# Kernel tuning notes

Hardware: AMD Instinct MI355X
Metric: run time of the kernel (lower is better)

## Reference

```python
import jax, jax.numpy as jnp
import numpy as np

N = 100000        # nodes
E = 1600000       # edges (avg degree 16)
D1, D2 = 512, 256 # omic feature dims
H = 64            # hidden_dim
C = 4             # num_classes


def setup_inputs() -> dict:
    key = jax.random.key(0)
    ks = jax.random.split(key, 13)
    s = 0.05  # param scale
    return {
        "x_omic1": jax.random.normal(ks[0], (N, D1), dtype=jnp.float32),
        "x_omic2": jax.random.normal(ks[1], (N, D2), dtype=jnp.float32),
        "edge_index": jax.random.randint(ks[2], (2, E), 0, N, dtype=jnp.int32),
        # GCNConv weights/biases, branch 1 (omic1)
        "W1a": jax.random.normal(ks[3], (D1, H), dtype=jnp.float32) * s,
        "b1a": jnp.zeros((H,), dtype=jnp.float32),
        "W2a": jax.random.normal(ks[4], (H, H), dtype=jnp.float32) * s,
        "b2a": jnp.zeros((H,), dtype=jnp.float32),
        # branch 2 (omic2)
        "W1b": jax.random.normal(ks[5], (D2, H), dtype=jnp.float32) * s,
        "b1b": jnp.zeros((H,), dtype=jnp.float32),
        "W2b": jax.random.normal(ks[6], (H, H), dtype=jnp.float32) * s,
        "b2b": jnp.zeros((H,), dtype=jnp.float32),
        # final classifier
        "Wfc": jax.random.normal(ks[7], (2 * H, C), dtype=jnp.float32) * s,
        "bfc": jnp.zeros((C,), dtype=jnp.float32),
    }


def reference(x_omic1, x_omic2, edge_index, W1a, b1a, W2a, b2a,
              W1b, b1b, W2b, b2b, Wfc, bfc):
    n = x_omic1.shape[0]
    # GCN normalization with self-loops: A_hat = A + I, norm = d^-1/2 d^-1/2
    loop = jnp.arange(n, dtype=edge_index.dtype)
    src = jnp.concatenate([edge_index[0], loop])
    dst = jnp.concatenate([edge_index[1], loop])
    deg = jax.ops.segment_sum(jnp.ones_like(src, dtype=x_omic1.dtype), dst,
                              num_segments=n)
    dinv = jnp.where(deg > 0, jax.lax.rsqrt(jnp.maximum(deg, 1.0)), 0.0)
    norm = dinv[src] * dinv[dst]  # [E+N]

    def gcn(x, W, b):
        h = x @ W                              # dense linear [n, H]
        msg = h[src] * norm[:, None]           # gather + scale
        return jax.ops.segment_sum(msg, dst, num_segments=n) + b

    # dropout is identity in eval mode
    x1 = jax.nn.elu(gcn(x_omic1, W1a, b1a))
    x1 = jax.nn.elu(gcn(x1, W2a, b2a))
    x2 = jax.nn.elu(gcn(x_omic2, W1b, b1b))
    x2 = jax.nn.elu(gcn(x2, W2b, b2b))
    x = jnp.concatenate([x1, x2], axis=1)      # [n, 2H]
    return x @ Wfc + bfc
```

## Files before the change

kernel.cpp:

```cpp
#include <hip/hip_runtime.h>
#include <hip/hip_bf16.h>
#include <math.h>


#define H 64
#define BCAP 16384

static inline int ceil_div(int a, int b) { return (a + b - 1) / b; }

typedef __attribute__((ext_vector_type(8))) short short8_t;
typedef __attribute__((ext_vector_type(4))) float f32x4;

__device__ inline unsigned short f2bf_rne(float f) {
    unsigned u = __float_as_uint(f);
    u += 0x7fffu + ((u >> 16) & 1u);
    return (unsigned short)(u >> 16);
}
__device__ inline unsigned pk_bf(float a, float b) {
    return (unsigned)f2bf_rne(a) | ((unsigned)f2bf_rne(b) << 16);
}
__device__ inline float2 bf2x(unsigned w) {
    float2 r;
    r.x = __uint_as_float(w << 16);
    r.y = __uint_as_float(w & 0xffff0000u);
    return r;
}
union V8 { uint4 u4; unsigned u[4]; short8_t s; };

__global__ __launch_bounds__(256) void bucket_scatter_kernel(
        const int* __restrict__ src, const int* __restrict__ dst,
        int* __restrict__ cursor, unsigned* __restrict__ bucketed,
        int E, int nbkt) {
    __shared__ int lcnt[512];
    __shared__ int lbase[512];
    const int t = threadIdx.x;
    for (int b = t; b < nbkt; b += 256) lcnt[b] = 0;
    __syncthreads();

    unsigned val[8];
    int bkt[8], lpos[8];
    const int e0 = blockIdx.x * 2048;
#pragma unroll
    for (int k = 0; k < 8; ++k) {
        int e = e0 + k * 256 + t;
        bkt[k] = -1;
        if (e < E) {
            int s = src[e];
            int d = dst[e];
            int b = d >> 8;
            val[k] = (unsigned)s | ((unsigned)(d & 255) << 17);
            bkt[k] = b;
            lpos[k] = atomicAdd(&lcnt[b], 1);
        }
    }
    __syncthreads();
    for (int b = t; b < nbkt; b += 256) {
        int c = lcnt[b];
        lbase[b] = c > 0 ? atomicAdd(&cursor[b], c) : 0;
    }
    __syncthreads();
#pragma unroll
    for (int k = 0; k < 8; ++k) {
        if (bkt[k] >= 0) {
            int p = lbase[bkt[k]] + lpos[k];
            if (p < BCAP)
                bucketed[(size_t)bkt[k] * BCAP + p] = val[k];
        }
    }
}

__global__ __launch_bounds__(512) void bucket_scan_kernel(
        const int* __restrict__ cursor, int* __restrict__ bucket_base,
        int* __restrict__ row_ptr, int nbkt, int N, int E) {
    __shared__ int s[512];
    const int t = threadIdx.x;
    int v = (t < nbkt) ? cursor[t] : 0;
    s[t] = v;
    __syncthreads();
#pragma unroll
    for (int off = 1; off < 512; off <<= 1) {
        int u = (t >= off) ? s[t - off] : 0;
        __syncthreads();
        s[t] += u;
        __syncthreads();
    }
    if (t < nbkt) bucket_base[t] = s[t] - v;
    if (t == 0) row_ptr[N] = E;
}

__global__ __launch_bounds__(256) void bucket_csr_kernel(
        const unsigned* __restrict__ bucketed, const int* __restrict__ cursor,
        const int* __restrict__ bucket_base, int* __restrict__ csr_src,
        int* __restrict__ row_ptr, float* __restrict__ dinv, int N) {
    __shared__ int dcnt[256];
    __shared__ int dbase[256];
    __shared__ int dcur[256];
    const int t = threadIdx.x;
    const int b = blockIdx.x;
    const int cnt = min(cursor[b], BCAP);
    const int base = bucket_base[b];
    const unsigned* bed = bucketed + (size_t)b * BCAP;

    dcnt[t] = 0;
    __syncthreads();
    for (int i = t; i < cnt; i += 256) {
        unsigned v = bed[i];
        atomicAdd(&dcnt[v >> 17], 1);
    }
    __syncthreads();
    int myc = dcnt[t];
    int acc = myc;
    dbase[t] = acc;
    __syncthreads();
#pragma unroll
    for (int off = 1; off < 256; off <<= 1) {
        int u = (t >= off) ? dbase[t - off] : 0;
        __syncthreads();
        dbase[t] += u;
        __syncthreads();
    }
    int excl = dbase[t] - myc;
    dcur[t] = excl;
    int node = b * 256 + t;
    if (node < N) {
        row_ptr[node] = base + excl;
        dinv[node] = rsqrtf((float)myc + 1.0f);
    }
    __syncthreads();
    for (int i = t; i < cnt; i += 256) {
        unsigned v = bed[i];
        int dl = v >> 17;
        int p = atomicAdd(&dcur[dl], 1);
        csr_src[base + p] = (int)(v & 0x1FFFFu);
    }
}

__global__ __launch_bounds__(256) void wfrag_kernel(const float* __restrict__ W,
                                                    uint4* __restrict__ frag, int K) {
    int t = blockIdx.x * 256 + threadIdx.x;
    int total = (K >> 5) * 256;
    if (t >= total) return;
    int lane = t & 63, nt = (t >> 6) & 3, ks = t >> 8;
    int nl = lane & 15, q = lane >> 4;
    float hi[8], lo[8];
#pragma unroll
    for (int j = 0; j < 8; ++j) {
        float w = W[(size_t)(ks * 32 + q * 8 + j) * 64 + nt * 16 + nl];
        unsigned hb = f2bf_rne(w);
        float hf = __uint_as_float(((unsigned)hb) << 16);
        hi[j] = hf;
        lo[j] = w - hf;
    }
    V8 vh, vl;
#pragma unroll
    for (int j = 0; j < 4; ++j) {
        vh.u[j] = pk_bf(hi[2 * j], hi[2 * j + 1]);
        vl.u[j] = pk_bf(lo[2 * j], lo[2 * j + 1]);
    }
    size_t base = (size_t)((ks * 4 + nt) * 2) * 64 + lane;
    frag[base] = vh.u4;
    frag[base + 64] = vl.u4;
}

__global__ __launch_bounds__(256) void gemm_l1_kernel(const float* __restrict__ X,
                                                      const uint4* __restrict__ wf,
                                                      unsigned* __restrict__ Hout,
                                                      int M, int K) {
    const int tid = threadIdx.x;
    const int w = tid >> 6, l = tid & 63;
    const int m = l & 15, q = l >> 4;
    const int tile = blockIdx.x * 64 + w * 16;
    int row = tile + m;
    int rowc = row < M ? row : M - 1;
    const float* Xr = X + (size_t)rowc * K;

    f32x4 acc[4];
#pragma unroll
    for (int nt = 0; nt < 4; ++nt) acc[nt] = (f32x4){0.f, 0.f, 0.f, 0.f};

    const int ksteps = K >> 5;
    for (int ks = 0; ks < ksteps; ++ks) {
        const float4 f0 = *(const float4*)&Xr[ks * 32 + q * 8];
        const float4 f1 = *(const float4*)&Xr[ks * 32 + q * 8 + 4];
        float xs[8] = {f0.x, f0.y, f0.z, f0.w, f1.x, f1.y, f1.z, f1.w};
        V8 ah, al;
#pragma unroll
        for (int j = 0; j < 4; ++j) {
            float a = xs[2 * j], b = xs[2 * j + 1];
            unsigned ha = f2bf_rne(a), hb = f2bf_rne(b);
            float fa = __uint_as_float(ha << 16);
            float fb = __uint_as_float(hb << 16);
            ah.u[j] = ha | (hb << 16);
            al.u[j] = pk_bf(a - fa, b - fb);
        }
        const uint4* base = wf + (size_t)(ks * 4) * 2 * 64 + l;
#pragma unroll
        for (int nt = 0; nt < 4; ++nt) {
            V8 bh, bl;
            bh.u4 = base[(size_t)(nt * 2) * 64];
            bl.u4 = base[(size_t)(nt * 2 + 1) * 64];
            acc[nt] = __builtin_amdgcn_mfma_f32_16x16x32_bf16(ah.s, bh.s, acc[nt], 0, 0, 0);
            acc[nt] = __builtin_amdgcn_mfma_f32_16x16x32_bf16(al.s, bh.s, acc[nt], 0, 0, 0);
            acc[nt] = __builtin_amdgcn_mfma_f32_16x16x32_bf16(ah.s, bl.s, acc[nt], 0, 0, 0);
        }
    }

    const int rbase = tile + q * 4;
#pragma unroll
    for (int nt = 0; nt < 4; ++nt) {
#pragma unroll
        for (int i = 0; i < 4; ++i) {
            float f = acc[nt][i];
            float fo = __shfl_xor(f, 1, 64);
            int r = rbase + i;
            if (((l & 1) == 0) && r < M)
                Hout[(size_t)r * 32 + nt * 8 + (m >> 1)] = pk_bf(f, fo);
        }
    }
}

__global__ __launch_bounds__(256) void gemm_l2_kernel(const uint4* __restrict__ Xb,
                                                      const uint4* __restrict__ wf,
                                                      unsigned* __restrict__ Hout,
                                                      int M) {
    const int tid = threadIdx.x;
    const int w = tid >> 6, l = tid & 63;
    const int m = l & 15, q = l >> 4;
    const int tile = blockIdx.x * 64 + w * 16;
    int row = tile + m;
    int rowc = row < M ? row : M - 1;

    f32x4 acc[4];
#pragma unroll
    for (int nt = 0; nt < 4; ++nt) acc[nt] = (f32x4){0.f, 0.f, 0.f, 0.f};

#pragma unroll
    for (int ks = 0; ks < 2; ++ks) {
        V8 av;
        av.u4 = Xb[(size_t)rowc * 8 + ks * 4 + q];
        const uint4* base = wf + (size_t)(ks * 4) * 2 * 64 + l;
#pragma unroll
        for (int nt = 0; nt < 4; ++nt) {
            V8 bh, bl;
            bh.u4 = base[(size_t)(nt * 2) * 64];
            bl.u4 = base[(size_t)(nt * 2 + 1) * 64];
            acc[nt] = __builtin_amdgcn_mfma_f32_16x16x32_bf16(av.s, bh.s, acc[nt], 0, 0, 0);
            acc[nt] = __builtin_amdgcn_mfma_f32_16x16x32_bf16(av.s, bl.s, acc[nt], 0, 0, 0);
        }
    }

    const int rbase = tile + q * 4;
#pragma unroll
    for (int nt = 0; nt < 4; ++nt) {
#pragma unroll
        for (int i = 0; i < 4; ++i) {
            float f = acc[nt][i];
            float fo = __shfl_xor(f, 1, 64);
            int r = rbase + i;
            if (((l & 1) == 0) && r < M)
                Hout[(size_t)r * 32 + nt * 8 + (m >> 1)] = pk_bf(f, fo);
        }
    }
}

__global__ __launch_bounds__(256) void agg2_kernel(const unsigned* __restrict__ h1,
                                                   const unsigned* __restrict__ h2,
                                                   const float* __restrict__ dinv,
                                                   const int* __restrict__ row_ptr,
                                                   const int* __restrict__ csr_src,
                                                   const float* __restrict__ b1,
                                                   const float* __restrict__ b2,
                                                   unsigned* __restrict__ o1,
                                                   unsigned* __restrict__ o2,
                                                   const float* __restrict__ Wfc,
                                                   const float* __restrict__ bfc,
                                                   float* __restrict__ out, int n) {
    const int tid  = threadIdx.x;
    const int lane = tid & 63;
    const int wave = tid >> 6;
    const int half = lane >> 5;
    const int l    = lane & 31;
    const int hb   = half << 5;
    const int node = blockIdx.x * 8 + wave * 2 + half;
    const bool active = (node < n);

    int r0 = 0, r1 = 0;
    float di = 0.f;
    if (active) { r0 = row_ptr[node]; r1 = row_ptr[node + 1]; di = dinv[node]; }
    const float di2 = di * di;
    const int rowoff = node * 32 + l;

    float2 acc1 = make_float2(0.f, 0.f), acc2 = make_float2(0.f, 0.f);
    if (active) {
        float2 s1 = bf2x(h1[rowoff]);
        float2 s2 = bf2x(h2[rowoff]);
        acc1.x = s1.x * di2; acc1.y = s1.y * di2;
        acc2.x = s2.x * di2; acc2.y = s2.y * di2;
    }

    for (int base = r0; base < r1; base += 32) {
        int cnt = r1 - base;
        if (cnt > 32) cnt = 32;
        int j = base + (l < cnt ? l : cnt - 1);
        int sj = csr_src[j];
        float dsj = dinv[sj];
#pragma unroll 4
        for (int t = 0; t < cnt; ++t) {
            int s    = __shfl(sj, hb | t, 64);
            float nr = __shfl(dsj, hb | t, 64) * di;
            float2 g1 = bf2x(h1[s * 32 + l]);
            float2 g2 = bf2x(h2[s * 32 + l]);
            acc1.x = fmaf(g1.x, nr, acc1.x);
            acc1.y = fmaf(g1.y, nr, acc1.y);
            acc2.x = fmaf(g2.x, nr, acc2.x);
            acc2.y = fmaf(g2.y, nr, acc2.y);
        }
    }

    float2 bv1 = ((const float2*)b1)[l];
    float2 bv2 = ((const float2*)b2)[l];
    float2 v1, v2;
    v1.x = acc1.x + bv1.x; v1.y = acc1.y + bv1.y;
    v2.x = acc2.x + bv2.x; v2.y = acc2.y + bv2.y;
    v1.x = v1.x > 0.f ? v1.x : (expf(v1.x) - 1.f);
    v1.y = v1.y > 0.f ? v1.y : (expf(v1.y) - 1.f);
    v2.x = v2.x > 0.f ? v2.x : (expf(v2.x) - 1.f);
    v2.y = v2.y > 0.f ? v2.y : (expf(v2.y) - 1.f);

    if (Wfc == nullptr) {
        if (active) {
            o1[rowoff] = pk_bf(v1.x, v1.y);
            o2[rowoff] = pk_bf(v2.x, v2.y);
        }
        return;
    }

    const float* Wp1 = &Wfc[(2 * l) * 4];
    const float* Wp2 = &Wfc[(H + 2 * l) * 4];
    float a[4];
#pragma unroll
    for (int c = 0; c < 4; ++c)
        a[c] = v1.x * Wp1[c] + v1.y * Wp1[4 + c] + v2.x * Wp2[c] + v2.y * Wp2[4 + c];
#pragma unroll
    for (int off = 16; off > 0; off >>= 1) {
#pragma unroll
        for (int c = 0; c < 4; ++c)
            a[c] += __shfl_down(a[c], off, 64);
    }
    if (l == 0 && active) {
#pragma unroll
        for (int c = 0; c < 4; ++c)
            out[(size_t)node * 4 + c] = a[c] + bfc[c];
    }
}

extern "C" void kernel_launch(void* const* d_in, const int* in_sizes, int n_in,
                              void* d_out, int out_size, void* d_ws, size_t ws_size,
                              hipStream_t stream) {
    const float* x_omic1 = (const float*)d_in[0];
    const float* x_omic2 = (const float*)d_in[1];
    const int*   eidx    = (const int*)d_in[2];
    const float* W1a = (const float*)d_in[3];
    const float* b1a = (const float*)d_in[4];
    const float* W2a = (const float*)d_in[5];
    const float* b2a = (const float*)d_in[6];
    const float* W1b = (const float*)d_in[7];
    const float* b1b = (const float*)d_in[8];
    const float* W2b = (const float*)d_in[9];
    const float* b2b = (const float*)d_in[10];
    const float* Wfc = (const float*)d_in[11];
    const float* bfc = (const float*)d_in[12];
    float* out = (float*)d_out;

    const int D1 = 512, D2 = 256;
    const int N = in_sizes[0] / D1;
    const int E = in_sizes[2] / 2;
    const int* src = eidx;
    const int* dst = eidx + E;
    const int nbkt = ceil_div(N, 256);

    size_t off = 0;
    auto alloc = [&](size_t elems) { size_t o = off; off += (elems + 3) & ~(size_t)3; return o; };
    float*    base_f = (float*)d_ws;
    int*      base_i = (int*)d_ws;
    unsigned* base_u = (unsigned*)d_ws;
    float*    dinv     = base_f + alloc(N);
    int*      row_ptr  = base_i + alloc(N + 1);
    int*      cursor   = base_i + alloc(512);
    int*      bkbase   = base_i + alloc(512);
    unsigned* bucketed = base_u + alloc((size_t)nbkt * BCAP);
    int*      csr_src  = base_i + alloc(E);
    unsigned* h1bf     = base_u + alloc((size_t)N * 32);
    unsigned* h2bf     = base_u + alloc((size_t)N * 32);
    unsigned* x1bf     = base_u + alloc((size_t)N * 32);
    unsigned* x2bf     = base_u + alloc((size_t)N * 32);
    uint4*    wf1a = (uint4*)(base_u + alloc((D1 / 32) * 2 * 256 * 4));
    uint4*    wf1b = (uint4*)(base_u + alloc((D2 / 32) * 2 * 256 * 4));
    uint4*    wf2a = (uint4*)(base_u + alloc((H  / 32) * 2 * 256 * 4));
    uint4*    wf2b = (uint4*)(base_u + alloc((H  / 32) * 2 * 256 * 4));

    dim3 blk(256);
    dim3 grid_agg(ceil_div(N, 8));
    dim3 grid_gemm(ceil_div(N, 64));

    hipMemsetAsync(cursor, 0, 512 * sizeof(int), stream);
    bucket_scatter_kernel<<<ceil_div(E, 2048), blk, 0, stream>>>(src, dst, cursor,
                                                                 bucketed, E, nbkt);
    bucket_scan_kernel<<<1, 512, 0, stream>>>(cursor, bkbase, row_ptr, nbkt, N, E);
    bucket_csr_kernel<<<nbkt, blk, 0, stream>>>(bucketed, cursor, bkbase,
                                                csr_src, row_ptr, dinv, N);

    wfrag_kernel<<<ceil_div((D1 / 32) * 256, 256), blk, 0, stream>>>(W1a, wf1a, D1);
    wfrag_kernel<<<ceil_div((D2 / 32) * 256, 256), blk, 0, stream>>>(W1b, wf1b, D2);
    wfrag_kernel<<<ceil_div((H  / 32) * 256, 256), blk, 0, stream>>>(W2a, wf2a, H);
    wfrag_kernel<<<ceil_div((H  / 32) * 256, 256), blk, 0, stream>>>(W2b, wf2b, H);

    gemm_l1_kernel<<<grid_gemm, blk, 0, stream>>>(x_omic1, wf1a, h1bf, N, D1);
    gemm_l1_kernel<<<grid_gemm, blk, 0, stream>>>(x_omic2, wf1b, h2bf, N, D2);
    agg2_kernel<<<grid_agg, blk, 0, stream>>>(h1bf, h2bf, dinv, row_ptr, csr_src,
                                              b1a, b1b, x1bf, x2bf,
                                              nullptr, nullptr, nullptr, N);
    gemm_l2_kernel<<<grid_gemm, blk, 0, stream>>>((const uint4*)x1bf, wf2a, h1bf, N);
    gemm_l2_kernel<<<grid_gemm, blk, 0, stream>>>((const uint4*)x2bf, wf2b, h2bf, N);
    agg2_kernel<<<grid_agg, blk, 0, stream>>>(h1bf, h2bf, dinv, row_ptr, csr_src,
                                              b2a, b2b, nullptr, nullptr,
                                              Wfc, bfc, out, N);
}
```

Measured before the change: 727.4 us.

## Merge small launches: fuse weight prep, bucket scan, and paired GEMM branches

```diff
diff --git a/kernel.cpp b/kernel.cpp
--- a/kernel.cpp
+++ b/kernel.cpp
@@ -69,37 +69,29 @@
     }
 }
 
-__global__ __launch_bounds__(512) void bucket_scan_kernel(
-        const int* __restrict__ cursor, int* __restrict__ bucket_base,
-        int* __restrict__ row_ptr, int nbkt, int N, int E) {
-    __shared__ int s[512];
-    const int t = threadIdx.x;
-    int v = (t < nbkt) ? cursor[t] : 0;
-    s[t] = v;
-    __syncthreads();
-#pragma unroll
-    for (int off = 1; off < 512; off <<= 1) {
-        int u = (t >= off) ? s[t - off] : 0;
-        __syncthreads();
-        s[t] += u;
-        __syncthreads();
-    }
-    if (t < nbkt) bucket_base[t] = s[t] - v;
-    if (t == 0) row_ptr[N] = E;
-}
-
 __global__ __launch_bounds__(256) void bucket_csr_kernel(
         const unsigned* __restrict__ bucketed, const int* __restrict__ cursor,
-        const int* __restrict__ bucket_base, int* __restrict__ csr_src,
-        int* __restrict__ row_ptr, float* __restrict__ dinv, int N) {
+        int* __restrict__ csr_src, int* __restrict__ row_ptr,
+        float* __restrict__ dinv, int N, int E) {
     __shared__ int dcnt[256];
     __shared__ int dbase[256];
     __shared__ int dcur[256];
     const int t = threadIdx.x;
     const int b = blockIdx.x;
+
+    int part = 0;
+    for (int i = t; i < b; i += 256) part += cursor[i];
+    dbase[t] = part;
+    __syncthreads();
+#pragma unroll
+    for (int off = 128; off > 0; off >>= 1) {
+        if (t < off) dbase[t] += dbase[t + off];
+        __syncthreads();
+    }
+    const int base = dbase[0];
     const int cnt = min(cursor[b], BCAP);
-    const int base = bucket_base[b];
     const unsigned* bed = bucketed + (size_t)b * BCAP;
+    if (b == 0 && t == 0) row_ptr[N] = E;
 
     dcnt[t] = 0;
     __syncthreads();
@@ -135,9 +127,24 @@
     }
 }
 
-__global__ __launch_bounds__(256) void wfrag_kernel(const float* __restrict__ W,
-                                                    uint4* __restrict__ frag, int K) {
-    int t = blockIdx.x * 256 + threadIdx.x;
+__global__ __launch_bounds__(256) void wfrag4_kernel(
+        const float* __restrict__ Wa, uint4* __restrict__ fa,
+        const float* __restrict__ Wb, uint4* __restrict__ fb,
+        const float* __restrict__ Wc, uint4* __restrict__ fc,
+        const float* __restrict__ Wd, uint4* __restrict__ fd,
+        int* __restrict__ cursor) {
+    const int bid = blockIdx.x;
+    if (bid == 0) {
+        cursor[threadIdx.x] = 0;
+        cursor[threadIdx.x + 256] = 0;
+    }
+    const float* W;
+    uint4* frag;
+    int K, t;
+    if (bid < 16)      { W = Wa; frag = fa; K = 512; t = bid * 256 + threadIdx.x; }
+    else if (bid < 24) { W = Wb; frag = fb; K = 256; t = (bid - 16) * 256 + threadIdx.x; }
+    else if (bid < 26) { W = Wc; frag = fc; K = 64;  t = (bid - 24) * 256 + threadIdx.x; }
+    else               { W = Wd; frag = fd; K = 64;  t = (bid - 26) * 256 + threadIdx.x; }
     int total = (K >> 5) * 256;
     if (t >= total) return;
     int lane = t & 63, nt = (t >> 6) & 3, ks = t >> 8;
@@ -162,14 +169,23 @@
     frag[base + 64] = vl.u4;
 }
 
-__global__ __launch_bounds__(256) void gemm_l1_kernel(const float* __restrict__ X,
-                                                      const uint4* __restrict__ wf,
-                                                      unsigned* __restrict__ Hout,
-                                                      int M, int K) {
+__global__ __launch_bounds__(256) void gemm_l1_kernel(
+        const float* __restrict__ XA, const uint4* __restrict__ wfA,
+        unsigned* __restrict__ HA, int KA,
+        const float* __restrict__ XB, const uint4* __restrict__ wfB,
+        unsigned* __restrict__ HB, int KB,
+        int M, int nblkA) {
+    const float* X;
+    const uint4* wf;
+    unsigned* Hout;
+    int K, blk;
+    if ((int)blockIdx.x < nblkA) { X = XA; wf = wfA; Hout = HA; K = KA; blk = blockIdx.x; }
+    else                         { X = XB; wf = wfB; Hout = HB; K = KB; blk = blockIdx.x - nblkA; }
+
     const int tid = threadIdx.x;
     const int w = tid >> 6, l = tid & 63;
     const int m = l & 15, q = l >> 4;
-    const int tile = blockIdx.x * 64 + w * 16;
+    const int tile = blk * 64 + w * 16;
     int row = tile + m;
     int rowc = row < M ? row : M - 1;
     const float* Xr = X + (size_t)rowc * K;
@@ -219,14 +235,23 @@
     }
 }
 
-__global__ __launch_bounds__(256) void gemm_l2_kernel(const uint4* __restrict__ Xb,
-                                                      const uint4* __restrict__ wf,
-                                                      unsigned* __restrict__ Hout,
-                                                      int M) {
+__global__ __launch_bounds__(256) void gemm_l2_kernel(
+        const uint4* __restrict__ XA, const uint4* __restrict__ wfA,
+        unsigned* __restrict__ HA,
+        const uint4* __restrict__ XB, const uint4* __restrict__ wfB,
+        unsigned* __restrict__ HB,
+        int M, int nblkA) {
+    const uint4* Xb;
+    const uint4* wf;
+    unsigned* Hout;
+    int blk;
+    if ((int)blockIdx.x < nblkA) { Xb = XA; wf = wfA; Hout = HA; blk = blockIdx.x; }
+    else                         { Xb = XB; wf = wfB; Hout = HB; blk = blockIdx.x - nblkA; }
+
     const int tid = threadIdx.x;
     const int w = tid >> 6, l = tid & 63;
     const int m = l & 15, q = l >> 4;
-    const int tile = blockIdx.x * 64 + w * 16;
+    const int tile = blk * 64 + w * 16;
     int row = tile + m;
     int rowc = row < M ? row : M - 1;
 
@@ -387,7 +412,6 @@
     float*    dinv     = base_f + alloc(N);
     int*      row_ptr  = base_i + alloc(N + 1);
     int*      cursor   = base_i + alloc(512);
-    int*      bkbase   = base_i + alloc(512);
     unsigned* bucketed = base_u + alloc((size_t)nbkt * BCAP);
     int*      csr_src  = base_i + alloc(E);
     unsigned* h1bf     = base_u + alloc((size_t)N * 32);
@@ -401,27 +425,22 @@
 
     dim3 blk(256);
     dim3 grid_agg(ceil_div(N, 8));
-    dim3 grid_gemm(ceil_div(N, 64));
-
-    hipMemsetAsync(cursor, 0, 512 * sizeof(int), stream);
+    const int nblk = ceil_div(N, 64);
+
+    wfrag4_kernel<<<28, blk, 0, stream>>>(W1a, wf1a, W1b, wf1b, W2a, wf2a,
+                                          W2b, wf2b, cursor);
     bucket_scatter_kernel<<<ceil_div(E, 2048), blk, 0, stream>>>(src, dst, cursor,
                                                                  bucketed, E, nbkt);
-    bucket_scan_kernel<<<1, 512, 0, stream>>>(cursor, bkbase, row_ptr, nbkt, N, E);
-    bucket_csr_kernel<<<nbkt, blk, 0, stream>>>(bucketed, cursor, bkbase,
-                                                csr_src, row_ptr, dinv, N);
-
-    wfrag_kernel<<<ceil_div((D1 / 32) * 256, 256), blk, 0, stream>>>(W1a, wf1a, D1);
-    wfrag_kernel<<<ceil_div((D2 / 32) * 256, 256), blk, 0, stream>>>(W1b, wf1b, D2);
-    wfrag_kernel<<<ceil_div((H  / 32) * 256, 256), blk, 0, stream>>>(W2a, wf2a, H);
-    wfrag_kernel<<<ceil_div((H  / 32) * 256, 256), blk, 0, stream>>>(W2b, wf2b, H);
-
-    gemm_l1_kernel<<<grid_gemm, blk, 0, stream>>>(x_omic1, wf1a, h1bf, N, D1);
-    gemm_l1_kernel<<<grid_gemm, blk, 0, stream>>>(x_omic2, wf1b, h2bf, N, D2);
+    bucket_csr_kernel<<<nbkt, blk, 0, stream>>>(bucketed, cursor, csr_src,
+                                                row_ptr, dinv, N, E);
+    gemm_l1_kernel<<<2 * nblk, blk, 0, stream>>>(x_omic1, wf1a, h1bf, D1,
+                                                 x_omic2, wf1b, h2bf, D2, N, nblk);
     agg2_kernel<<<grid_agg, blk, 0, stream>>>(h1bf, h2bf, dinv, row_ptr, csr_src,
                                               b1a, b1b, x1bf, x2bf,
                                               nullptr, nullptr, nullptr, N);
-    gemm_l2_kernel<<<grid_gemm, blk, 0, stream>>>((const uint4*)x1bf, wf2a, h1bf, N);
-    gemm_l2_kernel<<<grid_gemm, blk, 0, stream>>>((const uint4*)x2bf, wf2b, h2bf, N);
+    gemm_l2_kernel<<<2 * nblk, blk, 0, stream>>>((const uint4*)x1bf, wf2a, h1bf,
+                                                 (const uint4*)x2bf, wf2b, h2bf,
+                                                 N, nblk);
     agg2_kernel<<<grid_agg, blk, 0, stream>>>(h1bf, h2bf, dinv, row_ptr, csr_src,
                                               b2a, b2b, nullptr, nullptr,
                                               Wfc, bfc, out, N);
```

Result: faster. 699.4 us (-3.8%).
